# Kernel optimization log

Hardware: AMD Instinct MI355X
Metric: run time of the kernel (lower is better)

## Reference

```python
import jax, jax.numpy as jnp
import numpy as np

N_HEADS, N_LEVELS, N_POINTS = 8, 4, 4
D_MODEL, RNN, ENC, ATT_HID = 512, 512, 512, 512
D_HEAD = D_MODEL // N_HEADS  # att_feat_size = clip_context_dim / cap_nheads = 64
B = 1024
LEVEL_LENS = [1024, 512, 256, 128]
T_TOTAL = sum(LEVEL_LENS)


def setup_inputs() -> dict:
    key = jax.random.key(0)
    ks = jax.random.split(key, 24)
    s = 0.02  # weight init scale
    inp = {
        'xt': jax.random.normal(ks[0], (B, ENC), jnp.float32),
        'h0': jax.random.normal(ks[1], (2, B, RNN), jnp.float32),
        'c0': jax.random.normal(ks[2], (2, B, RNN), jnp.float32),
        'query': jax.random.normal(ks[3], (1, B, D_MODEL), jnp.float32),
        'reference_points': jax.random.uniform(ks[4], (1, B, N_LEVELS, 1), jnp.float32),
        'input_flatten': jax.random.normal(ks[5], (1, T_TOTAL, D_MODEL), jnp.float32),
        'input_spatial_shapes': jnp.asarray(LEVEL_LENS, jnp.int32),
        'input_level_start_index': jnp.asarray(np.cumsum([0] + LEVEL_LENS[:-1]), jnp.int32),
        'input_padding_mask': jnp.zeros((1, T_TOTAL), jnp.bool_),
        # MSDeformAttnCap params (query side sees cat(h, query) -> 2*D_MODEL)
        'W_value': jax.random.normal(ks[6], (D_MODEL, D_MODEL), jnp.float32) * s,
        'b_value': jnp.zeros((D_MODEL,), jnp.float32),
        'W_off': jax.random.normal(ks[7], (2 * D_MODEL, N_HEADS * N_LEVELS * N_POINTS), jnp.float32) * s,
        'b_off': jax.random.normal(ks[8], (N_HEADS * N_LEVELS * N_POINTS,), jnp.float32) * s,
        'W_attw': jax.random.normal(ks[9], (2 * D_MODEL, N_HEADS * N_LEVELS * N_POINTS), jnp.float32) * s,
        'b_attw': jnp.zeros((N_HEADS * N_LEVELS * N_POINTS,), jnp.float32),
        # additive SAT attention
        'W_ctx': jax.random.normal(ks[10], (D_HEAD, ATT_HID), jnp.float32) * s,
        'b_ctx': jnp.zeros((ATT_HID,), jnp.float32),
        'W_h2a': jax.random.normal(ks[11], (RNN, ATT_HID), jnp.float32) * s,
        'b_h2a': jnp.zeros((ATT_HID,), jnp.float32),
        'w_alpha': jax.random.normal(ks[12], (ATT_HID, 1), jnp.float32) * s,
        'b_alpha': jnp.zeros((1,), jnp.float32),
        # 2-layer LSTM, bias=False; input = ENC + 2*D_MODEL = 1536
        'Wih0': jax.random.normal(ks[13], (4 * RNN, ENC + 2 * D_MODEL), jnp.float32) * s,
        'Whh0': jax.random.normal(ks[14], (4 * RNN, RNN), jnp.float32) * s,
        'Wih1': jax.random.normal(ks[15], (4 * RNN, RNN), jnp.float32) * s,
        'Whh1': jax.random.normal(ks[16], (4 * RNN, RNN), jnp.float32) * s,
    }
    return inp


def _lstm_cell(x, h, c, Wih, Whh):
    g = x @ Wih.T + h @ Whh.T
    i, f, gg, o = jnp.split(g, 4, axis=-1)
    c2 = jax.nn.sigmoid(f) * c + jax.nn.sigmoid(i) * jnp.tanh(gg)
    h2 = jax.nn.sigmoid(o) * jnp.tanh(c2)
    return h2, c2


def reference(xt, h0, c0, query, reference_points, input_flatten,
              input_spatial_shapes, input_level_start_index, input_padding_mask,
              W_value, b_value, W_off, b_off, W_attw, b_attw,
              W_ctx, b_ctx, W_h2a, b_h2a, w_alpha, b_alpha,
              Wih0, Whh0, Wih1, Whh1):
    h_last = h0[-1]                                            # (B, RNN)
    jq = jnp.concatenate([h_last, query[0]], axis=-1)          # (B, 2D) joint query

    # ---- MSDeformAttnCap: value proj + 1D multi-level point sampling ----
    v = input_flatten[0] @ W_value + b_value                   # (T, D)
    v = jnp.where(input_padding_mask[0][:, None], 0.0, v)
    v = v.reshape(-1, N_HEADS, D_HEAD).transpose(1, 0, 2)     # (H, T, Dh)

    off = (jq @ W_off + b_off).reshape(B, N_HEADS, N_LEVELS, N_POINTS)
    aw = (jq @ W_attw + b_attw).reshape(B, N_HEADS, N_LEVELS * N_POINTS)
    aw = jax.nn.softmax(aw, axis=-1).reshape(B, N_HEADS, N_LEVELS, N_POINTS)

    Tf = input_spatial_shapes.astype(jnp.float32)              # (L,)
    ref = reference_points[0, :, :, 0]                          # (B, L) normalized centers
    loc = ref[:, None, :, None] + off / Tf[None, None, :, None]  # (B,H,L,P) in [0,1]

    # grid_sample(align_corners=False, zeros padding) linear interp along T
    x = loc * Tf[None, None, :, None] - 0.5
    x0 = jnp.floor(x)
    w1 = x - x0
    Ti = input_spatial_shapes[None, None, :, None]
    x0i = x0.astype(jnp.int32)
    valid0 = ((x0i >= 0) & (x0i < Ti)).astype(v.dtype)
    valid1 = ((x0i + 1 >= 0) & (x0i + 1 < Ti)).astype(v.dtype)
    start = input_level_start_index[None, None, :, None]
    i0 = jnp.clip(x0i, 0, Ti - 1) + start
    i1 = jnp.clip(x0i + 1, 0, Ti - 1) + start
    hids = jnp.arange(N_HEADS)[None, :, None, None]
    v0 = v[hids, i0]                                            # (B,H,L,P,Dh)
    v1 = v[hids, i1]
    samp = v0 * ((1.0 - w1) * valid0)[..., None] + v1 * (w1 * valid1)[..., None]
    # weighted sampled values, NOT summed over points (Cap variant)
    clip_feats = (samp * aw[..., None]).reshape(B, N_HEADS, N_LEVELS * N_POINTS, D_HEAD)

    # ---- additive SAT attention over the L*P sampled slots ----
    att_h = h_last @ W_h2a + b_h2a                              # (B, A)
    att = jnp.tanh(clip_feats @ W_ctx + b_ctx + att_h[:, None, None, :])  # (B,H,LP,A)
    dot = (att @ w_alpha)[..., 0] + b_alpha[0]                  # (B,H,LP)
    w = jax.nn.softmax(dot, axis=-1)
    att_res = jnp.einsum('bhp,bhpd->bhd', w, clip_feats).reshape(B, N_HEADS * D_HEAD)

    # ---- LSTM step (2 layers, bias=False, eval mode -> no dropout) ----
    x_in = jnp.concatenate([xt, att_res, query[0]], axis=-1)   # (B, ENC+2D)
    h1, c1 = _lstm_cell(x_in, h0[0], c0[0], Wih0, Whh0)
    h2, c2 = _lstm_cell(h1, h0[1], c0[1], Wih1, Whh1)
    h_new = jnp.stack([h1, h2])
    c_new = jnp.stack([c1, c2])
    return h2, h_new, c_new
```

## Files before the change

kernel.cpp:

```cpp
#include <hip/hip_runtime.h>
#include <math.h>


typedef __attribute__((ext_vector_type(8))) short          s16x8;
typedef __attribute__((ext_vector_type(8))) unsigned short u16x8;
typedef __attribute__((ext_vector_type(4))) float          f32x4;

#define LOG2E  1.4426950408889634f
#define LOG2E2 2.8853900817779268f

__device__ __forceinline__ float rcpf(float x) { return __builtin_amdgcn_rcpf(x); }
__device__ __forceinline__ float exp2f_fast(float x) { return __builtin_amdgcn_exp2f(x); }
__device__ __forceinline__ float sigf(float x) {
    return rcpf(1.0f + exp2f_fast(-x * LOG2E));
}
__device__ __forceinline__ float tanhf_fast(float x) {
    const float xc = fminf(fmaxf(x, -15.0f), 15.0f);
    const float e2 = exp2f_fast(xc * LOG2E2);
    return 1.0f - 2.0f * rcpf(e2 + 1.0f);
}
__device__ __forceinline__ unsigned short f2bf(float f) {
    unsigned u = __float_as_uint(f);
    u += 0x7FFF + ((u >> 16) & 1);
    return (unsigned short)(u >> 16);
}
__device__ __forceinline__ float bf2f(unsigned short h) {
    return __uint_as_float(((unsigned)h) << 16);
}
__device__ __forceinline__ void gld_lds16(const unsigned short* g, unsigned short* l) {
    __builtin_amdgcn_global_load_lds(
        (const __attribute__((address_space(1))) void*)g,
        (__attribute__((address_space(3))) void*)l, 16, 0, 0);
}

struct CvtJob { const float* src; unsigned short* dst; int sld, dld, cols, total, ilv; };
struct CvtJobs { CvtJob j[11]; };
__global__ __launch_bounds__(256) void cvt_bf16(CvtJobs cj) {
    const CvtJob jb = cj.j[blockIdx.y];
    const int i = (blockIdx.x * 256 + threadIdx.x) * 4;
    if (i >= jb.total) return;
    const int r = i / jb.cols, c = i - r * jb.cols;
    const int rd = jb.ilv ? (((r & 511) << 2) | (r >> 9)) : r;
    const float4 v4 = *(const float4*)&jb.src[(size_t)r * jb.sld + c];
    ushort4 o;
    o.x = f2bf(v4.x); o.y = f2bf(v4.y); o.z = f2bf(v4.z); o.w = f2bf(v4.w);
    *(ushort4*)&jb.dst[(size_t)rd * jb.dld + c] = o;
}

struct TJob { const float* src; unsigned short* dst; int N_, dld, K_, total; };
struct TJobs { TJob j[6]; };
__global__ __launch_bounds__(256) void tcvt_bf16(TJobs tj) {
    const TJob jb = tj.j[blockIdx.y];
    const int tilesN = jb.N_ >> 5, tilesK = jb.K_ >> 5;
    const int tile = blockIdx.x;
    if (tile >= tilesN * tilesK) return;
    const int tn0 = (tile % tilesN) << 5, tk0 = (tile / tilesN) << 5;
    __shared__ float lds[32][33];
    const int t = threadIdx.x;
    if (jb.src) {
#pragma unroll
        for (int q = 0; q < 4; ++q) {
            const int e = t + (q << 8);
            lds[e >> 5][e & 31] = jb.src[(size_t)(tk0 + (e >> 5)) * jb.N_ + tn0 + (e & 31)];
        }
        __syncthreads();
#pragma unroll
        for (int q = 0; q < 4; ++q) {
            const int e = t + (q << 8);
            const int n = e >> 5, k = e & 31;
            jb.dst[(size_t)(tn0 + n) * jb.dld + tk0 + k] = f2bf(lds[k][n]);
        }
    } else {
#pragma unroll
        for (int q = 0; q < 4; ++q) {
            const int e = t + (q << 8);
            jb.dst[(size_t)(tn0 + (e >> 5)) * jb.dld + tk0 + (e & 31)] = 0;
        }
    }
}

__global__ __launch_bounds__(768) void bias_cat3(const float* __restrict__ a,
                                                 const float* __restrict__ b,
                                                 const float* __restrict__ c,
                                                 float* __restrict__ dst) {
    const int t = threadIdx.x;
    dst[t] = (t < 128) ? a[t] : (t < 256 ? b[t - 128] : c[t - 256]);
}


#define STAGE_T(buf, k0) do { \
        gld_lds16(Ag1 + (k0), &As[buf][s1 * 8]); \
        gld_lds16(Ag2 + (k0), &As[buf][s2 * 8]); \
        gld_lds16(Bg1 + (k0), &Bs[buf][s1 * 8]); \
        gld_lds16(Bg2 + (k0), &Bs[buf][s2 * 8]); } while (0)

#define WAIT_INFL(t) do { \
        const int infl_ = nsteps - 1 - (t); \
        if (infl_ >= 2)      asm volatile("s_waitcnt vmcnt(8)" ::: "memory"); \
        else if (infl_ == 1) asm volatile("s_waitcnt vmcnt(4)" ::: "memory"); \
        else                 asm volatile("s_waitcnt vmcnt(0)" ::: "memory"); \
        __builtin_amdgcn_s_barrier(); } while (0)

struct GJob { const unsigned short* A; int lda; const unsigned short* B; int ldb;
              const float* bias; float* C; int ldc; int K; int nbx; int count; };
struct GJobs { GJob j[2]; };
__global__ __launch_bounds__(256) void sgemm2(GJobs gj) {
    __shared__ unsigned short As[4][64 * 64];
    __shared__ unsigned short Bs[4][64 * 64];

    int bid = blockIdx.x;
    GJob jb = gj.j[0];
    if (bid >= jb.count) { bid -= jb.count; jb = gj.j[1]; }
    const int bn = bid % jb.nbx, bm = bid / jb.nbx;
    const int lda = jb.lda, ldb = jb.ldb;

    const int tid = threadIdx.x;
    const int w = tid >> 6, lane = tid & 63;
    const int wr = w >> 1, wc = w & 1;
    const int lr = lane & 15, lg = lane >> 4;

    const int s1 = tid, s2 = tid + 256;
    const int r1 = s1 >> 3, c1 = ((s1 & 7) ^ (r1 & 7)) << 3;
    const int r2 = s2 >> 3, c2 = ((s2 & 7) ^ (r2 & 7)) << 3;
    const unsigned short* Ag1 = jb.A + (size_t)(bm * 64 + r1) * lda + c1;
    const unsigned short* Ag2 = jb.A + (size_t)(bm * 64 + r2) * lda + c2;
    const unsigned short* Bg1 = jb.B + (size_t)(bn * 64 + r1) * ldb + c1;
    const unsigned short* Bg2 = jb.B + (size_t)(bn * 64 + r2) * ldb + c2;

    f32x4 acc[2][2];
#pragma unroll
    for (int mt = 0; mt < 2; ++mt)
#pragma unroll
        for (int nt = 0; nt < 2; ++nt) acc[mt][nt] = (f32x4){0.f, 0.f, 0.f, 0.f};

    const int nsteps = jb.K >> 6;
    STAGE_T(0, 0);
    if (nsteps > 1) STAGE_T(1, 64);
    if (nsteps > 2) STAGE_T(2, 128);

    for (int t = 0; t < nsteps; ++t) {
        WAIT_INFL(t);
        if (t + 3 < nsteps) STAGE_T((t + 3) & 3, (t + 3) << 6);
        const unsigned short* Ab = &As[t & 3][0];
        const unsigned short* Bb = &Bs[t & 3][0];
        s16x8 a[2][2], bfr[2][2];
#pragma unroll
        for (int mt = 0; mt < 2; ++mt) {
            const int ar = wr * 32 + mt * 16 + lr;
#pragma unroll
            for (int ks = 0; ks < 2; ++ks)
                a[mt][ks] = *(const s16x8*)&Ab[(ar * 8 + ((ks * 4 + lg) ^ (ar & 7))) * 8];
        }
#pragma unroll
        for (int nt = 0; nt < 2; ++nt) {
            const int br = wc * 32 + nt * 16 + lr;
#pragma unroll
            for (int ks = 0; ks < 2; ++ks)
                bfr[nt][ks] = *(const s16x8*)&Bb[(br * 8 + ((ks * 4 + lg) ^ (br & 7))) * 8];
        }
#pragma unroll
        for (int ks = 0; ks < 2; ++ks)
#pragma unroll
            for (int mt = 0; mt < 2; ++mt)
#pragma unroll
                for (int nt = 0; nt < 2; ++nt)
                    acc[mt][nt] = __builtin_amdgcn_mfma_f32_16x16x32_bf16(
                        a[mt][ks], bfr[nt][ks], acc[mt][nt], 0, 0, 0);
    }
#pragma unroll
    for (int nt = 0; nt < 2; ++nt) {
        const int col = bn * 64 + wc * 32 + nt * 16 + lr;
        const float bb = jb.bias ? jb.bias[col] : 0.0f;
#pragma unroll
        for (int mt = 0; mt < 2; ++mt) {
            const int rbase = bm * 64 + wr * 32 + mt * 16 + lg * 4;
#pragma unroll
            for (int r = 0; r < 4; ++r)
                jb.C[(size_t)(rbase + r) * jb.ldc + col] = acc[mt][nt][r] + bb;
        }
    }
}

__global__ __launch_bounds__(256) void sgemm_lstm(
    const unsigned short* __restrict__ A, int lda,
    const unsigned short* __restrict__ B, int ldb,
    const float* __restrict__ c_in,
    float* __restrict__ h_a, float* __restrict__ h_b,
    unsigned short* __restrict__ hbf, int hbf_ld,
    float* __restrict__ c_out, int K)
{
    __shared__ unsigned short As[4][64 * 64];
    __shared__ unsigned short Bs[4][64 * 64];

    const int tid = threadIdx.x;
    const int w = tid >> 6, lane = tid & 63;
    const int wr = w >> 1, wc = w & 1;
    const int lr = lane & 15, lg = lane >> 4;
    const int bm = blockIdx.y, bn = blockIdx.x;

    const int s1 = tid, s2 = tid + 256;
    const int r1 = s1 >> 3, c1 = ((s1 & 7) ^ (r1 & 7)) << 3;
    const int r2 = s2 >> 3, c2 = ((s2 & 7) ^ (r2 & 7)) << 3;
    const unsigned short* Ag1 = A + (size_t)(bm * 64 + r1) * lda + c1;
    const unsigned short* Ag2 = A + (size_t)(bm * 64 + r2) * lda + c2;
    const unsigned short* Bg1 = B + (size_t)(bn * 64 + r1) * ldb + c1;
    const unsigned short* Bg2 = B + (size_t)(bn * 64 + r2) * ldb + c2;

    f32x4 acc[2][2];
#pragma unroll
    for (int mt = 0; mt < 2; ++mt)
#pragma unroll
        for (int nt = 0; nt < 2; ++nt) acc[mt][nt] = (f32x4){0.f, 0.f, 0.f, 0.f};

    const int nsteps = K >> 6;
    STAGE_T(0, 0);
    if (nsteps > 1) STAGE_T(1, 64);
    if (nsteps > 2) STAGE_T(2, 128);

    for (int t = 0; t < nsteps; ++t) {
        WAIT_INFL(t);
        if (t + 3 < nsteps) STAGE_T((t + 3) & 3, (t + 3) << 6);
        const unsigned short* Ab = &As[t & 3][0];
        const unsigned short* Bb = &Bs[t & 3][0];
        s16x8 a[2][2], bfr[2][2];
#pragma unroll
        for (int mt = 0; mt < 2; ++mt) {
            const int ar = wr * 32 + mt * 16 + lr;
#pragma unroll
            for (int ks = 0; ks < 2; ++ks)
                a[mt][ks] = *(const s16x8*)&Ab[(ar * 8 + ((ks * 4 + lg) ^ (ar & 7))) * 8];
        }
#pragma unroll
        for (int nt = 0; nt < 2; ++nt) {
            const int br = wc * 32 + nt * 16 + lr;
#pragma unroll
            for (int ks = 0; ks < 2; ++ks)
                bfr[nt][ks] = *(const s16x8*)&Bb[(br * 8 + ((ks * 4 + lg) ^ (br & 7))) * 8];
        }
#pragma unroll
        for (int ks = 0; ks < 2; ++ks)
#pragma unroll
            for (int mt = 0; mt < 2; ++mt)
#pragma unroll
                for (int nt = 0; nt < 2; ++nt)
                    acc[mt][nt] = __builtin_amdgcn_mfma_f32_16x16x32_bf16(
                        a[mt][ks], bfr[nt][ks], acc[mt][nt], 0, 0, 0);
    }
    const int gte  = lane & 3;
    const int base = lane & ~3;
#pragma unroll
    for (int nt = 0; nt < 2; ++nt) {
        const int col = bn * 64 + wc * 32 + nt * 16 + lr;
        const int u = col >> 2;
#pragma unroll
        for (int mt = 0; mt < 2; ++mt) {
            const int rbase = bm * 64 + wr * 32 + mt * 16 + lg * 4;
#pragma unroll
            for (int r = 0; r < 4; ++r) {
                const float vv = acc[mt][nt][r];
                const float a  = (gte == 2) ? tanhf_fast(vv) : sigf(vv);
                const float ai = __shfl(a, base + 0);
                const float af = __shfl(a, base + 1);
                const float ag = __shfl(a, base + 2);
                const float ao = __shfl(a, base + 3);
                const int row = rbase + r;
                const float c  = c_in[(size_t)row * 512 + u];
                const float c2 = af * c + ai * ag;
                const float h2 = ao * tanhf_fast(c2);
                if (gte == 0)      c_out[(size_t)row * 512 + u] = c2;
                else if (gte == 1) h_a[(size_t)row * 512 + u] = h2;
                else if (gte == 2) { if (h_b) h_b[(size_t)row * 512 + u] = h2; }
                else if (hbf)      hbf[(size_t)row * hbf_ld + u] = f2bf(h2);
            }
        }
    }
}
#undef STAGE_T
#undef WAIT_INFL

__global__ __launch_bounds__(256, 4) void fused_att(
    const float* __restrict__ v,
    const float* __restrict__ obat,
    const float* __restrict__ refp,
    const int*   __restrict__ shapes,
    const int*   __restrict__ starts,
    const unsigned short* __restrict__ Wb,
    const float* __restrict__ bctx,
    const float* __restrict__ walpha,
    unsigned short* __restrict__ attdst)
{
    __shared__ unsigned short cf[64 * 64];
    __shared__ float ba[512];
    __shared__ float wal[512];
    __shared__ float awb[64];
    __shared__ float dsum[64];
    __shared__ float dots4[4][64];

    const int b   = blockIdx.x >> 1;
    const int hh  = blockIdx.x & 1;
    const int tid = threadIdx.x;

    if (tid < 64) awb[tid] = obat[b * 768 + 128 + hh * 64 + tid];
    __syncthreads();
    if (tid < 4) {
        float mx = -1e30f;
        for (int i = 0; i < 16; ++i) mx = fmaxf(mx, awb[tid * 16 + i]);
        float sum = 0.f;
        for (int i = 0; i < 16; ++i) { float e = exp2f_fast((awb[tid * 16 + i] - mx) * LOG2E); awb[tid * 16 + i] = e; sum += e; }
        float inv = rcpf(sum);
        for (int i = 0; i < 16; ++i) awb[tid * 16 + i] *= inv;
    }
    __syncthreads();

    ba[tid]        = bctx[tid]       + obat[b * 768 + 256 + tid];
    ba[tid + 256]  = bctx[tid + 256] + obat[b * 768 + 512 + tid];
    wal[tid]       = walpha[tid];
    wal[tid + 256] = walpha[tid + 256];
    {
        const int pl  = tid >> 2;
        const int sub = tid & 3;
        const int d0  = sub * 16;
        const int pg  = hh * 64 + pl;
        const int h   = pg >> 4;
        const int l   = (pg & 15) >> 2;
        const int Tlen = shapes[l];
        const int st   = starts[l];
        const float T  = (float)Tlen;
        const float refv = refp[b * 4 + l];
        const float offv = obat[b * 768 + pg];
        const float awv  = awb[pl];
        const float x   = (refv + offv * rcpf(T)) * T - 0.5f;
        const float x0f = floorf(x);
        const float w1  = x - x0f;
        const int   x0  = (int)x0f;
        const float w0s = (x0 >= 0 && x0 < Tlen) ? (1.0f - w1) : 0.0f;
        const float w1s = (x0 + 1 >= 0 && x0 + 1 < Tlen) ? w1 : 0.0f;
        const int i0 = (min(max(x0, 0), Tlen - 1) + st) * 512 + h * 64;
        const int i1 = (min(max(x0 + 1, 0), Tlen - 1) + st) * 512 + h * 64;
        u16x8 o0, o1;
#pragma unroll
        for (int q = 0; q < 4; ++q) {
            const float4 a  = *(const float4*)&v[i0 + d0 + q * 4];
            const float4 bq = *(const float4*)&v[i1 + d0 + q * 4];
            unsigned short e0 = f2bf((a.x * w0s + bq.x * w1s) * awv);
            unsigned short e1 = f2bf((a.y * w0s + bq.y * w1s) * awv);
            unsigned short e2 = f2bf((a.z * w0s + bq.z * w1s) * awv);
            unsigned short e3 = f2bf((a.w * w0s + bq.w * w1s) * awv);
            if (q == 0) { o0[0] = e0; o0[1] = e1; o0[2] = e2; o0[3] = e3; }
            if (q == 1) { o0[4] = e0; o0[5] = e1; o0[6] = e2; o0[7] = e3; }
            if (q == 2) { o1[0] = e0; o1[1] = e1; o1[2] = e2; o1[3] = e3; }
            if (q == 3) { o1[4] = e0; o1[5] = e1; o1[6] = e2; o1[7] = e3; }
        }
        const int c0 = (sub * 2)     ^ (pl & 7);
        const int c1 = (sub * 2 + 1) ^ (pl & 7);
        *(u16x8*)&cf[pl * 64 + c0 * 8] = o0;
        *(u16x8*)&cf[pl * 64 + c1 * 8] = o1;
    }
    __syncthreads();

    {
        const int wn   = tid >> 6, lane = tid & 63;
        const int lr   = lane & 15, lg = lane >> 4;

        s16x8 afrag[4][2];
#pragma unroll
        for (int mt = 0; mt < 4; ++mt) {
            const int row = mt * 16 + lr;
#pragma unroll
            for (int ks = 0; ks < 2; ++ks) {
                const int ch = (ks * 4 + lg) ^ (row & 7);
                afrag[mt][ks] = *(const s16x8*)&cf[row * 64 + ch * 8];
            }
        }
        f32x4 part[4];
#pragma unroll
        for (int mt = 0; mt < 4; ++mt) part[mt] = (f32x4){0.f, 0.f, 0.f, 0.f};

#pragma clang loop unroll(disable)
        for (int nt = 0; nt < 8; ++nt) {
            const int col = (wn * 8 + nt) * 16 + lr;
            const s16x8 b0 = *(const s16x8*)&Wb[col * 64 + lg * 8];
            const s16x8 b1 = *(const s16x8*)&Wb[col * 64 + 32 + lg * 8];
            const float bav = ba[col], wav = wal[col];
#pragma unroll
            for (int mt = 0; mt < 4; ++mt) {
                f32x4 acc = {0.f, 0.f, 0.f, 0.f};
                acc = __builtin_amdgcn_mfma_f32_16x16x32_bf16(afrag[mt][0], b0, acc, 0, 0, 0);
                acc = __builtin_amdgcn_mfma_f32_16x16x32_bf16(afrag[mt][1], b1, acc, 0, 0, 0);
#pragma unroll
                for (int r = 0; r < 4; ++r)
                    part[mt][r] += tanhf_fast(acc[r] + bav) * wav;
            }
        }
#pragma unroll
        for (int mt = 0; mt < 4; ++mt) {
#pragma unroll
            for (int r = 0; r < 4; ++r) {
                float s = part[mt][r];
                s += __shfl_xor(s, 1); s += __shfl_xor(s, 2);
                s += __shfl_xor(s, 4); s += __shfl_xor(s, 8);
                if (lr == 0) dots4[wn][mt * 16 + lg * 4 + r] = s;
            }
        }
    }
    __syncthreads();
    if (tid < 64)
        dsum[tid] = dots4[0][tid] + dots4[1][tid] + dots4[2][tid] + dots4[3][tid];
    __syncthreads();

    if (tid < 4) {
        float mx = -1e30f;
        for (int i = 0; i < 16; ++i) mx = fmaxf(mx, dsum[tid * 16 + i]);
        float sum = 0.f;
        for (int i = 0; i < 16; ++i) { float e = exp2f_fast((dsum[tid * 16 + i] - mx) * LOG2E); dsum[tid * 16 + i] = e; sum += e; }
        float inv = rcpf(sum);
        for (int i = 0; i < 16; ++i) dsum[tid * 16 + i] *= inv;
    }
    __syncthreads();

    {
        const int hl = tid >> 6, d = tid & 63;
        const int ch = d >> 3, e = d & 7;
        float s = 0.f;
#pragma unroll
        for (int p = 0; p < 16; ++p) {
            const int row = hl * 16 + p;
            s += dsum[hl * 16 + p] * bf2f(cf[row * 64 + ((ch ^ (row & 7)) * 8) + e]);
        }
        attdst[(size_t)b * 2048 + hh * 256 + tid] = f2bf(s);
    }
}

extern "C" void kernel_launch(void* const* d_in, const int* in_sizes, int n_in,
                              void* d_out, int out_size, void* d_ws, size_t ws_size,
                              hipStream_t stream) {
    const float* xt     = (const float*)d_in[0];
    const float* h0     = (const float*)d_in[1];
    const float* c0     = (const float*)d_in[2];
    const float* query  = (const float*)d_in[3];
    const float* refp   = (const float*)d_in[4];
    const float* inflat = (const float*)d_in[5];
    const int*   shapes = (const int*)d_in[6];
    const int*   starts = (const int*)d_in[7];
    const float* Wv     = (const float*)d_in[9];
    const float* bv     = (const float*)d_in[10];
    const float* Woff   = (const float*)d_in[11];
    const float* boff   = (const float*)d_in[12];
    const float* Wattw  = (const float*)d_in[13];
    const float* battw  = (const float*)d_in[14];
    const float* Wctx   = (const float*)d_in[15];
    const float* bctx   = (const float*)d_in[16];
    const float* Wh2a   = (const float*)d_in[17];
    const float* bh2a   = (const float*)d_in[18];
    const float* walpha = (const float*)d_in[19];
    const float* Wih0   = (const float*)d_in[21];
    const float* Whh0   = (const float*)d_in[22];
    const float* Wih1   = (const float*)d_in[23];
    const float* Whh1   = (const float*)d_in[24];

    float* out = (float*)d_out;
    float* ws  = (float*)d_ws;

    float*          v     = ws;
    float*          obat  = ws + 983040;
    unsigned short* Acat  = (unsigned short*)(ws + 1769472);
    unsigned short* Bcat0 = (unsigned short*)(ws + 2818048);
    unsigned short* Ainf  = (unsigned short*)(ws + 4915200);
    unsigned short* Wvt   = (unsigned short*)(ws + 5406720);
    unsigned short* Wcat  = (unsigned short*)(ws + 5537792);
    unsigned short* Ahq   = (unsigned short*)(ws + 5931008);
    unsigned short* Wb    = (unsigned short*)(ws + 6455296);
    float*          bcat  = ws + 6471680;
    unsigned short* Ag1   = (unsigned short*)(ws + 7012352);
    unsigned short* Bcat1 = (unsigned short*)(ws + 7536640);

    const float* h00    = h0;
    const float* h_last = h0 + 524288;
    float* h1  = out + 524288;
    float* c1  = out + 1572864;
    float* h2a = out;
    float* h2b = out + 1048576;
    float* c2  = out + 2097152;

    { CvtJobs cj;
      cj.j[0]  = { xt,     Acat,          512,  2048, 512,  524288,  0 };
      cj.j[1]  = { query,  Acat + 1024,   512,  2048, 512,  524288,  0 };
      cj.j[2]  = { h00,    Acat + 1536,   512,  2048, 512,  524288,  0 };
      cj.j[3]  = { h_last, Ahq,           512,  1024, 512,  524288,  0 };
      cj.j[4]  = { query,  Ahq + 512,     512,  1024, 512,  524288,  0 };
      cj.j[5]  = { h_last, Ag1 + 512,     512,  1024, 512,  524288,  0 };
      cj.j[6]  = { Wih0,   Bcat0,         1536, 2048, 1536, 3145728, 1 };
      cj.j[7]  = { Whh0,   Bcat0 + 1536,  512,  2048, 512,  1048576, 1 };
      cj.j[8]  = { Wih1,   Bcat1,         512,  1024, 512,  1048576, 1 };
      cj.j[9]  = { Whh1,   Bcat1 + 512,   512,  1024, 512,  1048576, 1 };
      cj.j[10] = { inflat, Ainf,          512,  512,  512,  983040,  0 };
      cvt_bf16<<<dim3(3072, 11), 256, 0, stream>>>(cj); }
    { TJobs tj;
      tj.j[0] = { Wv,      Wvt,                     512, 512,  512, 0 };
      tj.j[1] = { Woff,    Wcat,                    128, 1024, 1024, 0 };
      tj.j[2] = { Wattw,   Wcat + 128 * 1024,       128, 1024, 1024, 0 };
      tj.j[3] = { Wh2a,    Wcat + 256 * 1024,       512, 1024, 512, 0 };
      tj.j[4] = { Wctx,    Wb,                      512, 64,   64,  0 };
      tj.j[5] = { nullptr, Wcat + 256 * 1024 + 512, 512, 1024, 512, 0 };
      tcvt_bf16<<<dim3(256, 6), 256, 0, stream>>>(tj); }
    bias_cat3<<<1, 768, 0, stream>>>(boff, battw, bh2a, bcat);

    { GJobs gj;
      gj.j[0] = { Ainf, 512,  Wvt,  512,  bv,   v,    512, 512,  8,  240 };
      gj.j[1] = { Ahq,  1024, Wcat, 1024, bcat, obat, 768, 1024, 12, 192 };
      sgemm2<<<432, 256, 0, stream>>>(gj); }

    fused_att<<<2048, 256, 0, stream>>>(v, obat, refp, shapes, starts,
                                        Wb, bctx, walpha, Acat + 512);

    sgemm_lstm<<<dim3(32, 16), 256, 0, stream>>>(Acat, 2048, Bcat0, 2048,
                                                 c0, h1, nullptr, Ag1, 1024, c1, 2048);
    sgemm_lstm<<<dim3(32, 16), 256, 0, stream>>>(Ag1, 1024, Bcat1, 1024,
                                                 c0 + 524288, h1 - 524288, h2b, nullptr, 0, c2, 1024);
}
```

Before: 113.7 us.

## Split-K LSTM GEMMs into two slices with separate bf16 reduce+cell kernel

The LSTM gate GEMMs now run as split-K with two K slices, doubling the block count from 512 to 1024. Each slice writes bf16 partial gate sums, and a new red_lstm kernel adds them and applies the LSTM cell. The pipeline depth drops from 4 to 3 LDS stages to cut shared memory and raise occupancy. The bias_cat3 launch is removed by selecting the bias inside the GEMM epilogue; in exchange there are two extra launches and partial gates are rounded to bf16, which costs precision.

Result: faster. 109.5 us (-3.7%).

```diff
diff --git a/kernel.cpp b/kernel.cpp
--- a/kernel.cpp
+++ b/kernel.cpp
@@ -79,14 +79,6 @@
     }
 }
 
-__global__ __launch_bounds__(768) void bias_cat3(const float* __restrict__ a,
-                                                 const float* __restrict__ b,
-                                                 const float* __restrict__ c,
-                                                 float* __restrict__ dst) {
-    const int t = threadIdx.x;
-    dst[t] = (t < 128) ? a[t] : (t < 256 ? b[t - 128] : c[t - 256]);
-}
-
 
 #define STAGE_T(buf, k0) do { \
         gld_lds16(Ag1 + (k0), &As[buf][s1 * 8]); \
@@ -94,15 +86,9 @@
         gld_lds16(Bg1 + (k0), &Bs[buf][s1 * 8]); \
         gld_lds16(Bg2 + (k0), &Bs[buf][s2 * 8]); } while (0)
 
-#define WAIT_INFL(t) do { \
-        const int infl_ = nsteps - 1 - (t); \
-        if (infl_ >= 2)      asm volatile("s_waitcnt vmcnt(8)" ::: "memory"); \
-        else if (infl_ == 1) asm volatile("s_waitcnt vmcnt(4)" ::: "memory"); \
-        else                 asm volatile("s_waitcnt vmcnt(0)" ::: "memory"); \
-        __builtin_amdgcn_s_barrier(); } while (0)
-
 struct GJob { const unsigned short* A; int lda; const unsigned short* B; int ldb;
-              const float* bias; float* C; int ldc; int K; int nbx; int count; };
+              const float* b0; const float* b1; const float* b2; int l0, l1;
+              float* C; int ldc; int K; int nbx; int count; };
 struct GJobs { GJob j[2]; };
 __global__ __launch_bounds__(256) void sgemm2(GJobs gj) {
     __shared__ unsigned short As[4][64 * 64];
@@ -139,7 +125,11 @@
     if (nsteps > 2) STAGE_T(2, 128);
 
     for (int t = 0; t < nsteps; ++t) {
-        WAIT_INFL(t);
+        const int infl = nsteps - 1 - t;
+        if (infl >= 2)      asm volatile("s_waitcnt vmcnt(8)" ::: "memory");
+        else if (infl == 1) asm volatile("s_waitcnt vmcnt(4)" ::: "memory");
+        else                asm volatile("s_waitcnt vmcnt(0)" ::: "memory");
+        __builtin_amdgcn_s_barrier();
         if (t + 3 < nsteps) STAGE_T((t + 3) & 3, (t + 3) << 6);
         const unsigned short* Ab = &As[t & 3][0];
         const unsigned short* Bb = &Bs[t & 3][0];
@@ -170,7 +160,10 @@
 #pragma unroll
     for (int nt = 0; nt < 2; ++nt) {
         const int col = bn * 64 + wc * 32 + nt * 16 + lr;
-        const float bb = jb.bias ? jb.bias[col] : 0.0f;
+        float bb;
+        if (col < jb.l0)      bb = jb.b0[col];
+        else if (col < jb.l1) bb = jb.b1[col - jb.l0];
+        else                  bb = jb.b2[col - jb.l1];
 #pragma unroll
         for (int mt = 0; mt < 2; ++mt) {
             const int rbase = bm * 64 + wr * 32 + mt * 16 + lg * 4;
@@ -181,30 +174,33 @@
     }
 }
 
-__global__ __launch_bounds__(256) void sgemm_lstm(
+__global__ __launch_bounds__(256) void sgemm_ks(
     const unsigned short* __restrict__ A, int lda,
     const unsigned short* __restrict__ B, int ldb,
-    const float* __restrict__ c_in,
-    float* __restrict__ h_a, float* __restrict__ h_b,
-    unsigned short* __restrict__ hbf, int hbf_ld,
-    float* __restrict__ c_out, int K)
+    unsigned short* __restrict__ gp0, unsigned short* __restrict__ gp1,
+    int Kslice)
 {
-    __shared__ unsigned short As[4][64 * 64];
-    __shared__ unsigned short Bs[4][64 * 64];
+    __shared__ unsigned short As[3][64 * 64];
+    __shared__ unsigned short Bs[3][64 * 64];
+
+    const int slice = blockIdx.x >> 9;
+    const int rblk  = blockIdx.x & 511;
+    const int bn = rblk & 31, bm = rblk >> 5;
+    const int koff = slice * Kslice;
+    unsigned short* Cp = slice ? gp1 : gp0;
 
     const int tid = threadIdx.x;
     const int w = tid >> 6, lane = tid & 63;
     const int wr = w >> 1, wc = w & 1;
     const int lr = lane & 15, lg = lane >> 4;
-    const int bm = blockIdx.y, bn = blockIdx.x;
 
     const int s1 = tid, s2 = tid + 256;
     const int r1 = s1 >> 3, c1 = ((s1 & 7) ^ (r1 & 7)) << 3;
     const int r2 = s2 >> 3, c2 = ((s2 & 7) ^ (r2 & 7)) << 3;
-    const unsigned short* Ag1 = A + (size_t)(bm * 64 + r1) * lda + c1;
-    const unsigned short* Ag2 = A + (size_t)(bm * 64 + r2) * lda + c2;
-    const unsigned short* Bg1 = B + (size_t)(bn * 64 + r1) * ldb + c1;
-    const unsigned short* Bg2 = B + (size_t)(bn * 64 + r2) * ldb + c2;
+    const unsigned short* Ag1 = A + (size_t)(bm * 64 + r1) * lda + koff + c1;
+    const unsigned short* Ag2 = A + (size_t)(bm * 64 + r2) * lda + koff + c2;
+    const unsigned short* Bg1 = B + (size_t)(bn * 64 + r1) * ldb + koff + c1;
+    const unsigned short* Bg2 = B + (size_t)(bn * 64 + r2) * ldb + koff + c2;
 
     f32x4 acc[2][2];
 #pragma unroll
@@ -212,16 +208,21 @@
 #pragma unroll
         for (int nt = 0; nt < 2; ++nt) acc[mt][nt] = (f32x4){0.f, 0.f, 0.f, 0.f};
 
-    const int nsteps = K >> 6;
+    const int nsteps = Kslice >> 6;
     STAGE_T(0, 0);
     if (nsteps > 1) STAGE_T(1, 64);
-    if (nsteps > 2) STAGE_T(2, 128);
 
     for (int t = 0; t < nsteps; ++t) {
-        WAIT_INFL(t);
-        if (t + 3 < nsteps) STAGE_T((t + 3) & 3, (t + 3) << 6);
-        const unsigned short* Ab = &As[t & 3][0];
-        const unsigned short* Bb = &Bs[t & 3][0];
+        const int infl = nsteps - 1 - t;
+        if (infl >= 1) asm volatile("s_waitcnt vmcnt(4)" ::: "memory");
+        else           asm volatile("s_waitcnt vmcnt(0)" ::: "memory");
+        __builtin_amdgcn_s_barrier();
+        if (t + 2 < nsteps) {
+            const int bw = (t + 2) % 3;
+            STAGE_T(bw, (t + 2) << 6);
+        }
+        const unsigned short* Ab = &As[t % 3][0];
+        const unsigned short* Bb = &Bs[t % 3][0];
         s16x8 a[2][2], bfr[2][2];
 #pragma unroll
         for (int mt = 0; mt < 2; ++mt) {
@@ -246,37 +247,44 @@
                     acc[mt][nt] = __builtin_amdgcn_mfma_f32_16x16x32_bf16(
                         a[mt][ks], bfr[nt][ks], acc[mt][nt], 0, 0, 0);
     }
-    const int gte  = lane & 3;
-    const int base = lane & ~3;
 #pragma unroll
     for (int nt = 0; nt < 2; ++nt) {
         const int col = bn * 64 + wc * 32 + nt * 16 + lr;
-        const int u = col >> 2;
 #pragma unroll
         for (int mt = 0; mt < 2; ++mt) {
             const int rbase = bm * 64 + wr * 32 + mt * 16 + lg * 4;
 #pragma unroll
-            for (int r = 0; r < 4; ++r) {
-                const float vv = acc[mt][nt][r];
-                const float a  = (gte == 2) ? tanhf_fast(vv) : sigf(vv);
-                const float ai = __shfl(a, base + 0);
-                const float af = __shfl(a, base + 1);
-                const float ag = __shfl(a, base + 2);
-                const float ao = __shfl(a, base + 3);
-                const int row = rbase + r;
-                const float c  = c_in[(size_t)row * 512 + u];
-                const float c2 = af * c + ai * ag;
-                const float h2 = ao * tanhf_fast(c2);
-                if (gte == 0)      c_out[(size_t)row * 512 + u] = c2;
-                else if (gte == 1) h_a[(size_t)row * 512 + u] = h2;
-                else if (gte == 2) { if (h_b) h_b[(size_t)row * 512 + u] = h2; }
-                else if (hbf)      hbf[(size_t)row * hbf_ld + u] = f2bf(h2);
-            }
+            for (int r = 0; r < 4; ++r)
+                Cp[(size_t)(rbase + r) * 2048 + col] = f2bf(acc[mt][nt][r]);
         }
     }
 }
 #undef STAGE_T
-#undef WAIT_INFL
+
+__global__ __launch_bounds__(256) void red_lstm(
+    const unsigned short* __restrict__ g0, const unsigned short* __restrict__ g1,
+    const float* __restrict__ c_in,
+    float* __restrict__ h_a, float* __restrict__ h_b,
+    unsigned short* __restrict__ hbf, int hbf_ld,
+    float* __restrict__ c_out)
+{
+    const int id = blockIdx.x * 256 + threadIdx.x;
+    const int row = id >> 9, u = id & 511;
+    const size_t off = (size_t)row * 2048 + u * 4;
+    const ushort4 p0 = *(const ushort4*)&g0[off];
+    const ushort4 p1 = *(const ushort4*)&g1[off];
+    const float gi = bf2f(p0.x) + bf2f(p1.x);
+    const float gf = bf2f(p0.y) + bf2f(p1.y);
+    const float gg = bf2f(p0.z) + bf2f(p1.z);
+    const float go = bf2f(p0.w) + bf2f(p1.w);
+    const float c  = c_in[id];
+    const float c2 = sigf(gf) * c + sigf(gi) * tanhf_fast(gg);
+    const float h2 = sigf(go) * tanhf_fast(c2);
+    h_a[id] = h2;
+    if (h_b) h_b[id] = h2;
+    if (hbf) hbf[(size_t)row * hbf_ld + u] = f2bf(h2);
+    c_out[id] = c2;
+}
 
 __global__ __launch_bounds__(256, 4) void fused_att(
     const float* __restrict__ v,
@@ -470,9 +478,10 @@
     unsigned short* Wcat  = (unsigned short*)(ws + 5537792);
     unsigned short* Ahq   = (unsigned short*)(ws + 5931008);
     unsigned short* Wb    = (unsigned short*)(ws + 6455296);
-    float*          bcat  = ws + 6471680;
     unsigned short* Ag1   = (unsigned short*)(ws + 7012352);
     unsigned short* Bcat1 = (unsigned short*)(ws + 7536640);
+    unsigned short* gp0 = (unsigned short*)ws;
+    unsigned short* gp1 = (unsigned short*)(ws + 4915200);
 
     const float* h00    = h0;
     const float* h_last = h0 + 524288;
@@ -503,18 +512,19 @@
       tj.j[4] = { Wctx,    Wb,                      512, 64,   64,  0 };
       tj.j[5] = { nullptr, Wcat + 256 * 1024 + 512, 512, 1024, 512, 0 };
       tcvt_bf16<<<dim3(256, 6), 256, 0, stream>>>(tj); }
-    bias_cat3<<<1, 768, 0, stream>>>(boff, battw, bh2a, bcat);
 
     { GJobs gj;
-      gj.j[0] = { Ainf, 512,  Wvt,  512,  bv,   v,    512, 512,  8,  240 };
-      gj.j[1] = { Ahq,  1024, Wcat, 1024, bcat, obat, 768, 1024, 12, 192 };
+      gj.j[0] = { Ainf, 512,  Wvt,  512,  bv,   bv,    bv,   0,   0,
+                  v,    512, 512,  8,  240 };
+      gj.j[1] = { Ahq,  1024, Wcat, 1024, boff, battw, bh2a, 128, 256,
+                  obat, 768, 1024, 12, 192 };
       sgemm2<<<432, 256, 0, stream>>>(gj); }
 
     fused_att<<<2048, 256, 0, stream>>>(v, obat, refp, shapes, starts,
                                         Wb, bctx, walpha, Acat + 512);
 
-    sgemm_lstm<<<dim3(32, 16), 256, 0, stream>>>(Acat, 2048, Bcat0, 2048,
-                                                 c0, h1, nullptr, Ag1, 1024, c1, 2048);
-    sgemm_lstm<<<dim3(32, 16), 256, 0, stream>>>(Ag1, 1024, Bcat1, 1024,
-                                                 c0 + 524288, h1 - 524288, h2b, nullptr, 0, c2, 1024);
-}
+    sgemm_ks<<<1024, 256, 0, stream>>>(Acat, 2048, Bcat0, 2048, gp0, gp1, 1024);
+    red_lstm<<<2048, 256, 0, stream>>>(gp0, gp1, c0, h1, nullptr, Ag1, 1024, c1);
+    sgemm_ks<<<1024, 256, 0, stream>>>(Ag1, 1024, Bcat1, 1024, gp0, gp1, 512);
+    red_lstm<<<2048, 256, 0, stream>>>(gp0, gp1, c0 + 524288, h2a, h2b, nullptr, 0, c2);
+}
```
